# Kernel tuning notes

Measured on AMD Instinct MI355X. Metric: run time of the kernel, lower is better.

## Reference

```python
import jax, jax.numpy as jnp
import numpy as np
import math

jax.config.update("jax_enable_x64", True)  # match torch int64 hash arithmetic

# ---- module config (from init_kwargs defaults) ----
N_LEVELS = 16
F = 2                       # n_feat_per_entry
HASHMAP_SIZE = 2 ** 19      # T
BASE_RES = 16
MAX_RES = 512
ORIGIN = np.array([0.0, 0.0, 0.0], dtype=np.float32)
SIDE = 1.5
B = 1048576

PER_LEVEL_SCALE = math.exp(math.log(MAX_RES / BASE_RES) / (N_LEVELS - 1))


def _level_table():
    resolutions, offsets = [], []
    n_total = 0
    for i in range(N_LEVELS):
        offsets.append(n_total)
        res = math.floor(BASE_RES * PER_LEVEL_SCALE ** i)
        resolutions.append(res)
        n_total += min(HASHMAP_SIZE, (res + 1) ** 3)
    offsets.append(n_total)
    return resolutions, offsets, n_total

RESOLUTIONS, OFFSETS_TBL, N_TOTAL_EMBED = _level_table()

# 8 voxel corner offsets, order (z fastest) as in ArcNerf Volume
CORNER_OFF = jnp.array([[0, 0, 0], [0, 0, 1], [0, 1, 0], [0, 1, 1],
                        [1, 0, 0], [1, 0, 1], [1, 1, 0], [1, 1, 1]], dtype=jnp.int64)
PRIMES = jnp.array([1, 2654435761, 805459861], dtype=jnp.int64)


def setup_inputs() -> dict:
    key = jax.random.key(0)
    k1, k2 = jax.random.split(key)
    # points inside the volume cube centered at ORIGIN with side SIDE
    xyz = jax.random.uniform(k1, (B, 3), dtype=jnp.float32,
                             minval=-SIDE / 2 * 0.999, maxval=SIDE / 2 * 0.999)
    embeddings = jax.random.uniform(k2, (N_TOTAL_EMBED, F), dtype=jnp.float32,
                                    minval=-1e-4, maxval=1e-4)
    return {"xyz": xyz, "embeddings": embeddings}


def _hashgrid_encode(xyz, embeddings):
    min_c = jnp.asarray(ORIGIN - SIDE / 2.0, dtype=xyz.dtype)  # (3,)
    outs = [xyz]  # include_input=True
    for lvl in range(N_LEVELS):
        res = RESOLUTIONS[lvl]
        tsize = OFFSETS_TBL[lvl + 1] - OFFSETS_TBL[lvl]
        voxel_size = SIDE / res
        g = (xyz - min_c) / voxel_size                      # (B,3) grid coords
        vidx = jnp.floor(g).astype(jnp.int64)               # (B,3)
        valid = jnp.all((vidx >= 0) & (vidx < res), axis=-1)  # (B,)
        vidx_c = jnp.clip(vidx, 0, res - 1)
        t = g - vidx_c.astype(g.dtype)                      # (B,3) frac in voxel
        corners = vidx_c[:, None, :] + CORNER_OFF[None]     # (B,8,3)
        # trilinear weights: prod over dims of t (offset=1) or 1-t (offset=0)
        off_b = CORNER_OFF.astype(bool)[None]               # (1,8,3)
        w = jnp.prod(jnp.where(off_b, t[:, None, :], 1.0 - t[:, None, :]), axis=-1)  # (B,8)
        # fast_hash: xor of idx*primes, mod per-level table size, plus level offset
        h = (corners[..., 0] * PRIMES[0]) ^ (corners[..., 1] * PRIMES[1]) ^ (corners[..., 2] * PRIMES[2])
        h = h % tsize + OFFSETS_TBL[lvl]                    # (B,8)
        e = embeddings[h]                                   # (B,8,F) gather
        lvl_out = jnp.einsum('bk,bkf->bf', w.astype(e.dtype), e)  # (B,F)
        lvl_out = jnp.where(valid[:, None], lvl_out, 0.0)
        outs.append(lvl_out)
    return jnp.concatenate(outs, axis=-1)  # (B, 3 + L*F)


def reference(xyz, embeddings):
    return _hashgrid_encode(xyz, embeddings)
```

## Files before the change

### kernel.cpp

```cpp
#include <hip/hip_runtime.h>
#include <hip/hip_fp16.h>
#include <cmath>

#define NLVL 16
#define BLK  256
#define LDSL 3
#define QLO  3
#define QHI  7
#define PAIRL 8
#define NB_LDS 256
#define LT_CAP 17664

typedef float v2f __attribute__((ext_vector_type(2)));

#define FP8_SCALE     8192.0f
#define FP8_INV_SCALE (1.0f / 8192.0f)

struct HGParams {
    int    res[NLVL];
    int    tsize[NLVL];
    int    off[NLVL];
    float  vs[NLVL];
    double tinv[NLVL];
    int    hOff[NLVL];
    int    quadOff[NLVL];
    int    t8Off[LDSL];
};

__device__ __forceinline__ uint32_t mod_u41(uint64_t v, int ts, double tinv) {
    const uint32_t q = (uint32_t)((double)v * tinv);
    int32_t r = (int32_t)((uint32_t)v - q * (uint32_t)ts);
    if (r < 0) r += ts;
    else if (r >= ts) r -= ts;
    return (uint32_t)r;
}

__device__ __forceinline__ uint32_t hash_at(int x, int y, int z, int ts, double tinv) {
    if ((ts & (ts - 1)) == 0) {
        const uint32_t m = (uint32_t)ts - 1u;
        return ((uint32_t)x ^ ((uint32_t)y * 2654435761u) ^ ((uint32_t)z * 805459861u)) & m;
    }
    const uint64_t v = (uint64_t)(uint32_t)x
                     ^ ((uint64_t)(uint32_t)y * 2654435761ull)
                     ^ ((uint64_t)(uint32_t)z * 805459861ull);
    return mod_u41(v, ts, tinv);
}

__device__ __forceinline__ int pack_fp8_pair(float a, float b) {
    return __builtin_amdgcn_cvt_pk_fp8_f32(a * FP8_SCALE, b * FP8_SCALE, 0, false);
}

__device__ __forceinline__ uint32_t ext16(uint4 v, uint32_t e) {
    const uint32_t s = e >> 1;
    const uint32_t dw = (s == 0) ? v.x : (s == 1) ? v.y : (s == 2) ? v.z : v.w;
    return (dw >> ((e & 1u) << 4)) & 0xFFFFu;
}

__device__ __forceinline__ void geom(
    float x, float y, float z, int res, float vs,
    int& ix, int& iy, int& iz,
    float& wx0, float& wx1, float& wy0, float& wy1, float& wz0, float& wz1,
    bool& valid)
{
    const float gx = (x + 0.75f) / vs;
    const float gy = (y + 0.75f) / vs;
    const float gz = (z + 0.75f) / vs;
    ix = (int)floorf(gx); iy = (int)floorf(gy); iz = (int)floorf(gz);
    valid = (ix >= 0) & (iy >= 0) & (iz >= 0) &
            (ix < res) & (iy < res) & (iz < res);
    ix = min(max(ix, 0), res - 1);
    iy = min(max(iy, 0), res - 1);
    iz = min(max(iz, 0), res - 1);
    const float tx = gx - (float)ix, ty = gy - (float)iy, tz = gz - (float)iz;
    wx0 = 1.f - tx; wx1 = tx; wy0 = 1.f - ty; wy1 = ty; wz0 = 1.f - tz; wz1 = tz;
}

__global__ __launch_bounds__(BLK) void build_all(
    const float2* __restrict__ emb,
    uint16_t* __restrict__ t8, uint16_t* __restrict__ hp8,
    uint2* __restrict__ quads, uint32_t* __restrict__ pairs,
    HGParams p, int nT8, int nH8, int nQ, int nP)
{
    int id = blockIdx.x * BLK + threadIdx.x;

    if (id < nT8) {
        int l = 0;
        #pragma unroll
        for (int k = 1; k < LDSL; ++k) if (id >= p.t8Off[k]) l = k;
        const float2 e = emb[p.off[l] + (id - p.t8Off[l])];
        t8[id] = (uint16_t)pack_fp8_pair(e.x, e.y);
        return;
    }
    id -= nT8;
    if (id < nH8) {
        const int l = 9 + (id >> 19);
        const float2 e = emb[p.off[l] + (id & 0x7FFFF)];
        hp8[id] = (uint16_t)pack_fp8_pair(e.x, e.y);
        return;
    }
    id -= nH8;
    if (id < nQ) {
        int l = QLO;
        #pragma unroll
        for (int k = QLO + 1; k <= QHI; ++k) if (id >= p.quadOff[k]) l = k;
        const int local = id - p.quadOff[l];
        const int res = p.res[l], rp1 = res + 1, ts = p.tsize[l], off = p.off[l];
        const int zb   = local % res;
        const int rest = local / res;
        const int y    = rest % rp1;
        const int x    = rest / rp1;

        const float2 e00 = emb[off + hash_at(x,     y, zb,     ts, p.tinv[l])];
        const float2 e01 = emb[off + hash_at(x,     y, zb + 1, ts, p.tinv[l])];
        const float2 e10 = emb[off + hash_at(x + 1, y, zb,     ts, p.tinv[l])];
        const float2 e11 = emb[off + hash_at(x + 1, y, zb + 1, ts, p.tinv[l])];

        int w0 = pack_fp8_pair(e00.x, e00.y);
        w0 = __builtin_amdgcn_cvt_pk_fp8_f32(e01.x * FP8_SCALE, e01.y * FP8_SCALE, w0, true);
        int w1 = pack_fp8_pair(e10.x, e10.y);
        w1 = __builtin_amdgcn_cvt_pk_fp8_f32(e11.x * FP8_SCALE, e11.y * FP8_SCALE, w1, true);
        uint2 q; q.x = (uint32_t)w0; q.y = (uint32_t)w1;
        quads[id] = q;
        return;
    }
    id -= nQ;
    if (id < nP) {
        const int l = PAIRL;
        const int res = p.res[l], rp1 = res + 1, ts = p.tsize[l], off = p.off[l];
        const int zb   = id % res;
        const int rest = id / res;
        const int y    = rest % rp1;
        const int x    = rest / rp1;
        const float2 e0 = emb[off + hash_at(x, y, zb,     ts, p.tinv[l])];
        const float2 e1 = emb[off + hash_at(x, y, zb + 1, ts, p.tinv[l])];
        int w = pack_fp8_pair(e0.x, e0.y);
        w = __builtin_amdgcn_cvt_pk_fp8_f32(e1.x * FP8_SCALE, e1.y * FP8_SCALE, w, true);
        pairs[id] = (uint32_t)w;
    }
}

__global__ __launch_bounds__(BLK) void fused_gather(
    const float*    __restrict__ xyz,
    const uint16_t* __restrict__ t8,
    const uint16_t* __restrict__ hp8,
    const uint2*    __restrict__ quads,
    const uint32_t* __restrict__ pairs,
    uint16_t*       __restrict__ sc,
    HGParams p, int B, int PB)
{
    __shared__ uint16_t lt[LT_CAP];
    const int tid = threadIdx.x;

    if (blockIdx.x < LDSL * NB_LDS) {
        const int l     = blockIdx.x / NB_LDS;
        const int chunk = blockIdx.x - l * NB_LDS;
        const int res   = p.res[l];
        const int ts    = p.tsize[l];
        const float vs  = p.vs[l];
        const double tinv = p.tinv[l];

        for (int k = tid; k < ts; k += BLK)
            lt[k] = t8[p.t8Off[l] + k];
        __syncthreads();

        const int PTS  = B / NB_LDS;
        const int base = chunk * PTS;
        for (int ii = tid; ii < PTS; ii += BLK) {
            const int i = base + ii;
            const float x = xyz[3*i], y = xyz[3*i+1], z = xyz[3*i+2];
            int ix, iy, iz; float wx0,wx1,wy0,wy1,wz0,wz1; bool valid;
            geom(x, y, z, res, vs, ix, iy, iz, wx0,wx1,wy0,wy1,wz0,wz1, valid);

            uint32_t idx[8];
            idx[0] = hash_at(ix,   iy,   iz,   ts, tinv);
            idx[1] = hash_at(ix,   iy,   iz+1, ts, tinv);
            idx[2] = hash_at(ix,   iy+1, iz,   ts, tinv);
            idx[3] = hash_at(ix,   iy+1, iz+1, ts, tinv);
            idx[4] = hash_at(ix+1, iy,   iz,   ts, tinv);
            idx[5] = hash_at(ix+1, iy,   iz+1, ts, tinv);
            idx[6] = hash_at(ix+1, iy+1, iz,   ts, tinv);
            idx[7] = hash_at(ix+1, iy+1, iz+1, ts, tinv);

            float w[8];
            w[0]=wx0*wy0*wz0; w[1]=wx0*wy0*wz1; w[2]=wx0*wy1*wz0; w[3]=wx0*wy1*wz1;
            w[4]=wx1*wy0*wz0; w[5]=wx1*wy0*wz1; w[6]=wx1*wy1*wz0; w[7]=wx1*wy1*wz1;

            float f0 = 0.f, f1 = 0.f;
            #pragma unroll
            for (int c = 0; c < 8; ++c) {
                const v2f f = __builtin_amdgcn_cvt_pk_f32_fp8((int)(uint32_t)lt[idx[c]], false);
                f0 += w[c] * f.x; f1 += w[c] * f.y;
            }
            f0 *= FP8_INV_SCALE; f1 *= FP8_INV_SCALE;
            if (!valid) { f0 = 0.f; f1 = 0.f; }
            sc[((size_t)(i >> 8) * NLVL + l) * BLK + (i & 255)]
                = (uint16_t)pack_fp8_pair(f0, f1);
        }
        return;
    }

    const int bid = blockIdx.x - LDSL * NB_LDS;
    const int l  = 3 + bid / PB;
    const int pb = bid % PB;
    const int i  = pb * BLK + tid;
    if (i >= B) return;

    const float x = xyz[3*i], y = xyz[3*i+1], z = xyz[3*i+2];
    const int   res = p.res[l];
    int ix, iy, iz; float wx0,wx1,wy0,wy1,wz0,wz1; bool valid;
    geom(x, y, z, res, p.vs[l], ix, iy, iz, wx0,wx1,wy0,wy1,wz0,wz1, valid);

    float f0 = 0.f, f1 = 0.f;

    if (l <= QHI) {
        const int rp1 = res + 1;
        const uint32_t base = (uint32_t)p.quadOff[l];
        const uint32_t i00  = ((uint32_t)ix * rp1 + (uint32_t)iy) * (uint32_t)res
                              + (uint32_t)iz;
        const uint2 q0 = quads[base + i00];
        const uint2 q1 = quads[base + i00 + (uint32_t)res];

        #define ACCQ(q, wy) do {                                               \
            const v2f a0 = __builtin_amdgcn_cvt_pk_f32_fp8((int)(q).x, false);  \
            const v2f a1 = __builtin_amdgcn_cvt_pk_f32_fp8((int)(q).x, true);   \
            const v2f b0 = __builtin_amdgcn_cvt_pk_f32_fp8((int)(q).y, false);  \
            const v2f b1 = __builtin_amdgcn_cvt_pk_f32_fp8((int)(q).y, true);   \
            f0 += (wy) * (wx0 * (wz0*a0.x + wz1*a1.x) + wx1 * (wz0*b0.x + wz1*b1.x)); \
            f1 += (wy) * (wx0 * (wz0*a0.y + wz1*a1.y) + wx1 * (wz0*b0.y + wz1*b1.y)); \
        } while (0)
        ACCQ(q0, wy0);
        ACCQ(q1, wy1);
        #undef ACCQ
        f0 *= FP8_INV_SCALE; f1 *= FP8_INV_SCALE;
    } else if (l == PAIRL) {
        const int rp1 = res + 1;
        const uint32_t i00 = ((uint32_t)ix * rp1 + (uint32_t)iy) * (uint32_t)res
                             + (uint32_t)iz;
        const uint32_t q00 = pairs[i00];
        const uint32_t q01 = pairs[i00 + (uint32_t)res];
        const uint32_t q10 = pairs[i00 + (uint32_t)rp1 * (uint32_t)res];
        const uint32_t q11 = pairs[i00 + (uint32_t)rp1 * (uint32_t)res + (uint32_t)res];
        #define ACCP(q, wxy) do {                                           \
            const v2f a = __builtin_amdgcn_cvt_pk_f32_fp8((int)(q), false);  \
            const v2f b = __builtin_amdgcn_cvt_pk_f32_fp8((int)(q), true);   \
            f0 += (wxy) * (wz0 * a.x + wz1 * b.x);                          \
            f1 += (wxy) * (wz0 * a.y + wz1 * b.y);                          \
        } while (0)
        ACCP(q00, wx0 * wy0);
        ACCP(q01, wx0 * wy1);
        ACCP(q10, wx1 * wy0);
        ACCP(q11, wx1 * wy1);
        #undef ACCP
        f0 *= FP8_INV_SCALE; f1 *= FP8_INV_SCALE;
    } else {
        const uint16_t* __restrict__ tab = hp8 + (uint32_t)p.hOff[l];
        const uint32_t mask = 0x7FFFFu;
        const uint32_t x0 = (uint32_t)ix;
        const uint32_t d  = x0 ^ (x0 + 1u);
        const uint32_t hy0 = (uint32_t)iy * 2654435761u, hy1 = hy0 + 2654435761u;
        const uint32_t hz0 = (uint32_t)iz * 805459861u,  hz1 = hz0 + 805459861u;

        const float wyz[4] = { wy0*wz0, wy0*wz1, wy1*wz0, wy1*wz1 };
        const uint32_t hc[4] = {
            (x0 ^ hy0 ^ hz0) & mask, (x0 ^ hy0 ^ hz1) & mask,
            (x0 ^ hy1 ^ hz0) & mask, (x0 ^ hy1 ^ hz1) & mask };

        #pragma unroll
        for (int c = 0; c < 4; ++c) {
            const uint32_t h0 = hc[c];
            const uint32_t h1 = h0 ^ d;
            const uint4 v = *(const uint4*)(tab + (h0 & ~7u));
            const uint32_t e0 = ext16(v, h0 & 7u);
            uint32_t e1;
            if (d <= 7u) {
                e1 = ext16(v, h1 & 7u);
            } else {
                const uint4 v2 = *(const uint4*)(tab + (h1 & ~7u));
                e1 = ext16(v2, h1 & 7u);
            }
            const v2f a = __builtin_amdgcn_cvt_pk_f32_fp8((int)e0, false);
            const v2f b = __builtin_amdgcn_cvt_pk_f32_fp8((int)e1, false);
            f0 += wyz[c] * (wx0 * a.x + wx1 * b.x);
            f1 += wyz[c] * (wx0 * a.y + wx1 * b.y);
        }
        f0 *= FP8_INV_SCALE; f1 *= FP8_INV_SCALE;
    }

    if (!valid) { f0 = 0.f; f1 = 0.f; }
    sc[((size_t)pb * NLVL + l) * BLK + tid] = (uint16_t)pack_fp8_pair(f0, f1);
}

__global__ __launch_bounds__(BLK) void assemble_out(
    const float*    __restrict__ xyz,
    const uint16_t* __restrict__ sc,
    float*          __restrict__ out, int B)
{
    __shared__ float s_out[BLK * 35];
    const int tid = threadIdx.x;
    const int pb  = blockIdx.x;
    const int i   = pb * BLK + tid;

    if (i < B) {
        s_out[tid * 35 + 0] = xyz[3*i];
        s_out[tid * 35 + 1] = xyz[3*i+1];
        s_out[tid * 35 + 2] = xyz[3*i+2];
        const uint16_t* slab = sc + (size_t)pb * NLVL * BLK;
        #pragma unroll
        for (int l = 0; l < NLVL; ++l) {
            const v2f f = __builtin_amdgcn_cvt_pk_f32_fp8(
                (int)(uint32_t)slab[l * BLK + tid], false);
            s_out[tid * 35 + 3 + 2*l]     = f.x * FP8_INV_SCALE;
            s_out[tid * 35 + 3 + 2*l + 1] = f.y * FP8_INV_SCALE;
        }
    }
    __syncthreads();

    const int rows = min(B - pb * BLK, BLK);
    if (rows == BLK) {
        float4* __restrict__ o4 = (float4*)(out + (size_t)pb * (BLK * 35));
        const float4* s4 = (const float4*)s_out;
        for (int k = tid; k < (BLK * 35) / 4; k += BLK)
            o4[k] = s4[k];
    } else {
        const long long base = (long long)pb * (BLK * 35);
        const int tot = rows * 35;
        for (int k = tid; k < tot; k += BLK)
            out[base + k] = s_out[k];
    }
}

__global__ __launch_bounds__(BLK) void hashgrid_mono(
    const float*  __restrict__ xyz,
    const float2* __restrict__ emb,
    float*        __restrict__ out,
    HGParams p, int B)
{
    __shared__ float s_out[BLK * 35];
    const int tid = threadIdx.x;
    const int i   = blockIdx.x * BLK + tid;
    if (i < B) {
        const float x = xyz[3*i], y = xyz[3*i+1], z = xyz[3*i+2];
        s_out[tid*35] = x; s_out[tid*35+1] = y; s_out[tid*35+2] = z;
        for (int l = 0; l < NLVL; ++l) {
            const int res = p.res[l], ts = p.tsize[l];
            int ix, iy, iz; float wx0,wx1,wy0,wy1,wz0,wz1; bool valid;
            geom(x, y, z, res, p.vs[l], ix, iy, iz, wx0,wx1,wy0,wy1,wz0,wz1, valid);
            uint32_t idx[8];
            idx[0] = hash_at(ix,   iy,   iz,   ts, p.tinv[l]);
            idx[1] = hash_at(ix,   iy,   iz+1, ts, p.tinv[l]);
            idx[2] = hash_at(ix,   iy+1, iz,   ts, p.tinv[l]);
            idx[3] = hash_at(ix,   iy+1, iz+1, ts, p.tinv[l]);
            idx[4] = hash_at(ix+1, iy,   iz,   ts, p.tinv[l]);
            idx[5] = hash_at(ix+1, iy,   iz+1, ts, p.tinv[l]);
            idx[6] = hash_at(ix+1, iy+1, iz,   ts, p.tinv[l]);
            idx[7] = hash_at(ix+1, iy+1, iz+1, ts, p.tinv[l]);
            float w[8];
            w[0]=wx0*wy0*wz0; w[1]=wx0*wy0*wz1; w[2]=wx0*wy1*wz0; w[3]=wx0*wy1*wz1;
            w[4]=wx1*wy0*wz0; w[5]=wx1*wy0*wz1; w[6]=wx1*wy1*wz0; w[7]=wx1*wy1*wz1;
            float f0 = 0.f, f1 = 0.f;
            #pragma unroll
            for (int c = 0; c < 8; ++c) {
                const float2 e = emb[p.off[l] + idx[c]];
                f0 += w[c]*e.x; f1 += w[c]*e.y;
            }
            if (!valid) { f0 = 0.f; f1 = 0.f; }
            s_out[tid*35 + 3 + 2*l] = f0; s_out[tid*35 + 4 + 2*l] = f1;
        }
    }
    __syncthreads();
    const long long base = (long long)blockIdx.x * (BLK * 35);
    const int rows = min(B - blockIdx.x * BLK, BLK);
    for (int k = tid; k < rows * 35; k += BLK) out[base + k] = s_out[k];
}

extern "C" void kernel_launch(void* const* d_in, const int* in_sizes, int n_in,
                              void* d_out, int out_size, void* d_ws, size_t ws_size,
                              hipStream_t stream) {
    const float*  xyz = (const float*)d_in[0];
    const float2* emb = (const float2*)d_in[1];
    float*        out = (float*)d_out;
    const int B = in_sizes[0] / 3;

    HGParams p;
    const double scale = exp(log(512.0 / 16.0) / 15.0);
    int ntot = 0;
    for (int i = 0; i < NLVL; ++i) {
        p.off[i] = ntot;
        const int res = (int)floor(16.0 * pow(scale, (double)i));
        p.res[i] = res;
        const long long dense = (long long)(res + 1) * (res + 1) * (res + 1);
        const int ts = (int)(dense < 524288LL ? dense : 524288LL);
        p.tsize[i] = ts;
        ntot += ts;
        p.vs[i]   = (float)(1.5 / (double)res);
        p.tinv[i] = 1.0 / (double)ts;
    }

    const int PB = (B + BLK - 1) / BLK;

    int nT8 = 0, maxTs = 0;
    for (int l = 0; l < LDSL; ++l) {
        p.t8Off[l] = nT8; nT8 += p.tsize[l];
        maxTs = max(maxTs, p.tsize[l]);
    }

    int nQ = 0;
    for (int l = QLO; l <= QHI; ++l) {
        p.quadOff[l] = nQ;
        nQ += p.res[l] * (p.res[l] + 1) * p.res[l];
    }
    const int nP = (p.res[PAIRL] + 1) * (p.res[PAIRL] + 1) * p.res[PAIRL];

    int nH8 = 0;
    for (int l = 9; l < NLVL; ++l) { p.hOff[l] = nH8; nH8 += p.tsize[l]; }

    const size_t t8B = (((size_t)nT8 * 2) + 255) & ~(size_t)255;
    const size_t hpB = (((size_t)nH8 * 2) + 255) & ~(size_t)255;
    const size_t qB  = (((size_t)nQ  * 8) + 255) & ~(size_t)255;
    const size_t prB = (((size_t)nP  * 4) + 255) & ~(size_t)255;
    const size_t scB = (size_t)PB * NLVL * BLK * sizeof(uint16_t);
    const size_t need = t8B + hpB + qB + prB + scB;

    if (ws_size >= need && (B % NB_LDS) == 0 && (B % BLK) == 0 && maxTs <= LT_CAP) {
        uint16_t* t8    = (uint16_t*)d_ws;
        uint16_t* hp8   = (uint16_t*)((char*)d_ws + t8B);
        uint2*    quads = (uint2*)((char*)d_ws + t8B + hpB);
        uint32_t* pairs = (uint32_t*)((char*)d_ws + t8B + hpB + qB);
        uint16_t* sc    = (uint16_t*)((char*)d_ws + t8B + hpB + qB + prB);

        const int nBuild = nT8 + nH8 + nQ + nP;
        hipLaunchKernelGGL(build_all, dim3((nBuild + BLK - 1) / BLK), dim3(BLK),
                           0, stream, emb, t8, hp8, quads, pairs, p, nT8, nH8, nQ, nP);
        hipLaunchKernelGGL(fused_gather, dim3(LDSL * NB_LDS + (NLVL - 3) * PB), dim3(BLK),
                           0, stream, xyz, t8, hp8, quads, pairs, sc, p, B, PB);
        hipLaunchKernelGGL(assemble_out, dim3(PB), dim3(BLK),
                           0, stream, xyz, sc, out, B);
    } else {
        hipLaunchKernelGGL(hashgrid_mono, dim3(PB), dim3(BLK),
                           0, stream, xyz, emb, out, p, B);
    }
}
```

Baseline: 428.1 us.

## Replace LDS-resident coarse levels with per-voxel packed 8-corner global tables

Levels 0-5 now get a precomputed per-voxel table that packs all 8 corner embeddings as fp8 into one 16-byte entry. This replaces the old LDS-table path for levels 0-2 and the quad layout for levels 3-5. Each point at these levels then needs a single 16-byte gather instead of 8 LDS lookups with hashing or two quad loads, and the kernel drops the LDS fill, the sync and the special block split. The cost is a larger build step (8 embedding reads per voxel, about 8x storage for these levels) and more global-memory and cache traffic at the coarse levels, where the LDS path used to serve lookups.

```diff
diff --git a/kernel.cpp b/kernel.cpp
--- a/kernel.cpp
+++ b/kernel.cpp
@@ -4,12 +4,10 @@
 
 #define NLVL 16
 #define BLK  256
-#define LDSL 3
-#define QLO  3
+#define VOXHI 5
+#define QLO  6
 #define QHI  7
 #define PAIRL 8
-#define NB_LDS 256
-#define LT_CAP 17664
 
 typedef float v2f __attribute__((ext_vector_type(2)));
 
@@ -24,7 +22,7 @@
     double tinv[NLVL];
     int    hOff[NLVL];
     int    quadOff[NLVL];
-    int    t8Off[LDSL];
+    int    voxOff[VOXHI + 1];
 };
 
 __device__ __forceinline__ uint32_t mod_u41(uint64_t v, int ts, double tinv) {
@@ -77,21 +75,40 @@
 
 __global__ __launch_bounds__(BLK) void build_all(
     const float2* __restrict__ emb,
-    uint16_t* __restrict__ t8, uint16_t* __restrict__ hp8,
+    uint4* __restrict__ vox, uint16_t* __restrict__ hp8,
     uint2* __restrict__ quads, uint32_t* __restrict__ pairs,
-    HGParams p, int nT8, int nH8, int nQ, int nP)
+    HGParams p, int nV, int nH8, int nQ, int nP)
 {
     int id = blockIdx.x * BLK + threadIdx.x;
 
-    if (id < nT8) {
+    if (id < nV) {
         int l = 0;
         #pragma unroll
-        for (int k = 1; k < LDSL; ++k) if (id >= p.t8Off[k]) l = k;
-        const float2 e = emb[p.off[l] + (id - p.t8Off[l])];
-        t8[id] = (uint16_t)pack_fp8_pair(e.x, e.y);
+        for (int k = 1; k <= VOXHI; ++k) if (id >= p.voxOff[k]) l = k;
+        const int local = id - p.voxOff[l];
+        const int res = p.res[l], ts = p.tsize[l], off = p.off[l];
+        const int z    = local % res;
+        const int rest = local / res;
+        const int y    = rest % res;
+        const int x    = rest / res;
+
+        uint32_t w[4];
+        #pragma unroll
+        for (int dx = 0; dx < 2; ++dx)
+            #pragma unroll
+            for (int dy = 0; dy < 2; ++dy) {
+                const float2 e0 = emb[off + hash_at(x+dx, y+dy, z,   ts, p.tinv[l])];
+                const float2 e1 = emb[off + hash_at(x+dx, y+dy, z+1, ts, p.tinv[l])];
+                int wl = pack_fp8_pair(e0.x, e0.y);
+                wl = __builtin_amdgcn_cvt_pk_fp8_f32(e1.x * FP8_SCALE,
+                                                     e1.y * FP8_SCALE, wl, true);
+                w[dx * 2 + dy] = (uint32_t)wl;
+            }
+        uint4 q; q.x = w[0]; q.y = w[1]; q.z = w[2]; q.w = w[3];
+        vox[id] = q;
         return;
     }
-    id -= nT8;
+    id -= nV;
     if (id < nH8) {
         const int l = 9 + (id >> 19);
         const float2 e = emb[p.off[l] + (id & 0x7FFFF)];
@@ -101,8 +118,7 @@
     id -= nH8;
     if (id < nQ) {
         int l = QLO;
-        #pragma unroll
-        for (int k = QLO + 1; k <= QHI; ++k) if (id >= p.quadOff[k]) l = k;
+        if (id >= p.quadOff[QHI]) l = QHI;
         const int local = id - p.quadOff[l];
         const int res = p.res[l], rp1 = res + 1, ts = p.tsize[l], off = p.off[l];
         const int zb   = local % res;
@@ -141,67 +157,16 @@
 
 __global__ __launch_bounds__(BLK) void fused_gather(
     const float*    __restrict__ xyz,
-    const uint16_t* __restrict__ t8,
+    const uint4*    __restrict__ vox,
     const uint16_t* __restrict__ hp8,
     const uint2*    __restrict__ quads,
     const uint32_t* __restrict__ pairs,
     uint16_t*       __restrict__ sc,
     HGParams p, int B, int PB)
 {
-    __shared__ uint16_t lt[LT_CAP];
     const int tid = threadIdx.x;
-
-    if (blockIdx.x < LDSL * NB_LDS) {
-        const int l     = blockIdx.x / NB_LDS;
-        const int chunk = blockIdx.x - l * NB_LDS;
-        const int res   = p.res[l];
-        const int ts    = p.tsize[l];
-        const float vs  = p.vs[l];
-        const double tinv = p.tinv[l];
-
-        for (int k = tid; k < ts; k += BLK)
-            lt[k] = t8[p.t8Off[l] + k];
-        __syncthreads();
-
-        const int PTS  = B / NB_LDS;
-        const int base = chunk * PTS;
-        for (int ii = tid; ii < PTS; ii += BLK) {
-            const int i = base + ii;
-            const float x = xyz[3*i], y = xyz[3*i+1], z = xyz[3*i+2];
-            int ix, iy, iz; float wx0,wx1,wy0,wy1,wz0,wz1; bool valid;
-            geom(x, y, z, res, vs, ix, iy, iz, wx0,wx1,wy0,wy1,wz0,wz1, valid);
-
-            uint32_t idx[8];
-            idx[0] = hash_at(ix,   iy,   iz,   ts, tinv);
-            idx[1] = hash_at(ix,   iy,   iz+1, ts, tinv);
-            idx[2] = hash_at(ix,   iy+1, iz,   ts, tinv);
-            idx[3] = hash_at(ix,   iy+1, iz+1, ts, tinv);
-            idx[4] = hash_at(ix+1, iy,   iz,   ts, tinv);
-            idx[5] = hash_at(ix+1, iy,   iz+1, ts, tinv);
-            idx[6] = hash_at(ix+1, iy+1, iz,   ts, tinv);
-            idx[7] = hash_at(ix+1, iy+1, iz+1, ts, tinv);
-
-            float w[8];
-            w[0]=wx0*wy0*wz0; w[1]=wx0*wy0*wz1; w[2]=wx0*wy1*wz0; w[3]=wx0*wy1*wz1;
-            w[4]=wx1*wy0*wz0; w[5]=wx1*wy0*wz1; w[6]=wx1*wy1*wz0; w[7]=wx1*wy1*wz1;
-
-            float f0 = 0.f, f1 = 0.f;
-            #pragma unroll
-            for (int c = 0; c < 8; ++c) {
-                const v2f f = __builtin_amdgcn_cvt_pk_f32_fp8((int)(uint32_t)lt[idx[c]], false);
-                f0 += w[c] * f.x; f1 += w[c] * f.y;
-            }
-            f0 *= FP8_INV_SCALE; f1 *= FP8_INV_SCALE;
-            if (!valid) { f0 = 0.f; f1 = 0.f; }
-            sc[((size_t)(i >> 8) * NLVL + l) * BLK + (i & 255)]
-                = (uint16_t)pack_fp8_pair(f0, f1);
-        }
-        return;
-    }
-
-    const int bid = blockIdx.x - LDSL * NB_LDS;
-    const int l  = 3 + bid / PB;
-    const int pb = bid % PB;
+    const int l  = blockIdx.x / PB;
+    const int pb = blockIdx.x % PB;
     const int i  = pb * BLK + tid;
     if (i >= B) return;
 
@@ -212,14 +177,29 @@
 
     float f0 = 0.f, f1 = 0.f;
 
-    if (l <= QHI) {
+    #define ACCW(word, wxy) do {                                            \
+        const v2f a = __builtin_amdgcn_cvt_pk_f32_fp8((int)(word), false);   \
+        const v2f b = __builtin_amdgcn_cvt_pk_f32_fp8((int)(word), true);    \
+        f0 += (wxy) * (wz0 * a.x + wz1 * b.x);                              \
+        f1 += (wxy) * (wz0 * a.y + wz1 * b.y);                              \
+    } while (0)
+
+    if (l <= VOXHI) {
+        const uint32_t vi = ((uint32_t)ix * (uint32_t)res + (uint32_t)iy)
+                            * (uint32_t)res + (uint32_t)iz;
+        const uint4 q = vox[(uint32_t)p.voxOff[l] + vi];
+        ACCW(q.x, wx0 * wy0);
+        ACCW(q.y, wx0 * wy1);
+        ACCW(q.z, wx1 * wy0);
+        ACCW(q.w, wx1 * wy1);
+        f0 *= FP8_INV_SCALE; f1 *= FP8_INV_SCALE;
+    } else if (l <= QHI) {
         const int rp1 = res + 1;
         const uint32_t base = (uint32_t)p.quadOff[l];
         const uint32_t i00  = ((uint32_t)ix * rp1 + (uint32_t)iy) * (uint32_t)res
                               + (uint32_t)iz;
         const uint2 q0 = quads[base + i00];
         const uint2 q1 = quads[base + i00 + (uint32_t)res];
-
         #define ACCQ(q, wy) do {                                               \
             const v2f a0 = __builtin_amdgcn_cvt_pk_f32_fp8((int)(q).x, false);  \
             const v2f a1 = __builtin_amdgcn_cvt_pk_f32_fp8((int)(q).x, true);   \
@@ -240,17 +220,10 @@
         const uint32_t q01 = pairs[i00 + (uint32_t)res];
         const uint32_t q10 = pairs[i00 + (uint32_t)rp1 * (uint32_t)res];
         const uint32_t q11 = pairs[i00 + (uint32_t)rp1 * (uint32_t)res + (uint32_t)res];
-        #define ACCP(q, wxy) do {                                           \
-            const v2f a = __builtin_amdgcn_cvt_pk_f32_fp8((int)(q), false);  \
-            const v2f b = __builtin_amdgcn_cvt_pk_f32_fp8((int)(q), true);   \
-            f0 += (wxy) * (wz0 * a.x + wz1 * b.x);                          \
-            f1 += (wxy) * (wz0 * a.y + wz1 * b.y);                          \
-        } while (0)
-        ACCP(q00, wx0 * wy0);
-        ACCP(q01, wx0 * wy1);
-        ACCP(q10, wx1 * wy0);
-        ACCP(q11, wx1 * wy1);
-        #undef ACCP
+        ACCW(q00, wx0 * wy0);
+        ACCW(q01, wx0 * wy1);
+        ACCW(q10, wx1 * wy0);
+        ACCW(q11, wx1 * wy1);
         f0 *= FP8_INV_SCALE; f1 *= FP8_INV_SCALE;
     } else {
         const uint16_t* __restrict__ tab = hp8 + (uint32_t)p.hOff[l];
@@ -285,6 +258,7 @@
         }
         f0 *= FP8_INV_SCALE; f1 *= FP8_INV_SCALE;
     }
+    #undef ACCW
 
     if (!valid) { f0 = 0.f; f1 = 0.f; }
     sc[((size_t)pb * NLVL + l) * BLK + tid] = (uint16_t)pack_fp8_pair(f0, f1);
@@ -398,10 +372,10 @@
 
     const int PB = (B + BLK - 1) / BLK;
 
-    int nT8 = 0, maxTs = 0;
-    for (int l = 0; l < LDSL; ++l) {
-        p.t8Off[l] = nT8; nT8 += p.tsize[l];
-        maxTs = max(maxTs, p.tsize[l]);
+    int nV = 0;
+    for (int l = 0; l <= VOXHI; ++l) {
+        p.voxOff[l] = nV;
+        nV += p.res[l] * p.res[l] * p.res[l];
     }
 
     int nQ = 0;
@@ -414,25 +388,25 @@
     int nH8 = 0;
     for (int l = 9; l < NLVL; ++l) { p.hOff[l] = nH8; nH8 += p.tsize[l]; }
 
-    const size_t t8B = (((size_t)nT8 * 2) + 255) & ~(size_t)255;
-    const size_t hpB = (((size_t)nH8 * 2) + 255) & ~(size_t)255;
-    const size_t qB  = (((size_t)nQ  * 8) + 255) & ~(size_t)255;
-    const size_t prB = (((size_t)nP  * 4) + 255) & ~(size_t)255;
+    const size_t vB  = (((size_t)nV  * 16) + 255) & ~(size_t)255;
+    const size_t hpB = (((size_t)nH8 * 2)  + 255) & ~(size_t)255;
+    const size_t qB  = (((size_t)nQ  * 8)  + 255) & ~(size_t)255;
+    const size_t prB = (((size_t)nP  * 4)  + 255) & ~(size_t)255;
     const size_t scB = (size_t)PB * NLVL * BLK * sizeof(uint16_t);
-    const size_t need = t8B + hpB + qB + prB + scB;
-
-    if (ws_size >= need && (B % NB_LDS) == 0 && (B % BLK) == 0 && maxTs <= LT_CAP) {
-        uint16_t* t8    = (uint16_t*)d_ws;
-        uint16_t* hp8   = (uint16_t*)((char*)d_ws + t8B);
-        uint2*    quads = (uint2*)((char*)d_ws + t8B + hpB);
-        uint32_t* pairs = (uint32_t*)((char*)d_ws + t8B + hpB + qB);
-        uint16_t* sc    = (uint16_t*)((char*)d_ws + t8B + hpB + qB + prB);
-
-        const int nBuild = nT8 + nH8 + nQ + nP;
+    const size_t need = vB + hpB + qB + prB + scB;
+
+    if (ws_size >= need && (B % BLK) == 0) {
+        uint4*    vox   = (uint4*)d_ws;
+        uint16_t* hp8   = (uint16_t*)((char*)d_ws + vB);
+        uint2*    quads = (uint2*)((char*)d_ws + vB + hpB);
+        uint32_t* pairs = (uint32_t*)((char*)d_ws + vB + hpB + qB);
+        uint16_t* sc    = (uint16_t*)((char*)d_ws + vB + hpB + qB + prB);
+
+        const int nBuild = nV + nH8 + nQ + nP;
         hipLaunchKernelGGL(build_all, dim3((nBuild + BLK - 1) / BLK), dim3(BLK),
-                           0, stream, emb, t8, hp8, quads, pairs, p, nT8, nH8, nQ, nP);
-        hipLaunchKernelGGL(fused_gather, dim3(LDSL * NB_LDS + (NLVL - 3) * PB), dim3(BLK),
-                           0, stream, xyz, t8, hp8, quads, pairs, sc, p, B, PB);
+                           0, stream, emb, vox, hp8, quads, pairs, p, nV, nH8, nQ, nP);
+        hipLaunchKernelGGL(fused_gather, dim3(NLVL * PB), dim3(BLK),
+                           0, stream, xyz, vox, hp8, quads, pairs, sc, p, B, PB);
         hipLaunchKernelGGL(assemble_out, dim3(PB), dim3(BLK),
                            0, stream, xyz, sc, out, B);
     } else {
```

After: 418.4 us. 1.02x faster.
